# Optimization experiments

Measured on AMD Instinct MI355X. Metric: run time of the kernel, lower is better.

The kernel has to match this reference:

```python
import jax, jax.numpy as jnp
import numpy as np

NUM_NODES = 50000
DIM = 64
NUM_LAYERS = 2
NUM_EDGES = 800000
EPS = 1e-12


def _l2_normalize(x):
    # F.normalize(x, dim=1): x / max(||x||_2, eps)
    n = jnp.sqrt(jnp.sum(x * x, axis=1, keepdims=True))
    return x / jnp.maximum(n, EPS)


def _lgconv(x, src, dst):
    # PyG LGConv: symmetric gcn_norm without self-loops.
    # deg computed at target nodes; out[dst] += d^-1/2[src] * d^-1/2[dst] * x[src]
    ones = jnp.ones(src.shape[0], dtype=x.dtype)
    deg = jax.ops.segment_sum(ones, dst, num_segments=NUM_NODES)
    dinv = jnp.where(deg > 0, 1.0 / jnp.sqrt(jnp.where(deg > 0, deg, 1.0)), 0.0)
    norm = dinv[src] * dinv[dst]  # [E]
    msg = norm[:, None] * x[src]  # [E, D] gather + scale
    return jax.ops.segment_sum(msg, dst, num_segments=NUM_NODES)


def _propagate(x, edge_index):
    src, dst = edge_index[0], edge_index[1]
    for _ in range(NUM_LAYERS):
        x = _lgconv(x, src, dst)
    return _l2_normalize(x)


def setup_inputs() -> dict:
    key = jax.random.key(0)
    k1, k2, k3, k4 = jax.random.split(key, 4)
    x = jax.random.normal(k1, (NUM_NODES, DIM), dtype=jnp.float32)
    alpha = jnp.ones((3,), dtype=jnp.float32)
    ei_t = jax.random.randint(k2, (2, NUM_EDGES), 0, NUM_NODES, dtype=jnp.int32)
    ei_y = jax.random.randint(k3, (2, NUM_EDGES), 0, NUM_NODES, dtype=jnp.int32)
    ei_c = jax.random.randint(k4, (2, NUM_EDGES), 0, NUM_NODES, dtype=jnp.int32)
    return {"x": x, "alpha": alpha, "edge_index_title": ei_t,
            "edge_index_year": ei_y, "edge_index_cat": ei_c}


def reference(x, alpha, edge_index_title, edge_index_year, edge_index_cat):
    x = _l2_normalize(x)
    x_title = _propagate(x, edge_index_title)
    x_year = _propagate(x, edge_index_year)
    x_cat = _propagate(x, edge_index_cat)
    w = jax.nn.softmax(alpha, axis=0)
    w = jnp.clip(w, 0.0001, None)
    w = w / jnp.sum(w)
    return w[0] * x_title + w[1] * x_year + w[2] * x_cat
```

## Files before the change

### kernel.cpp

```cpp
#include <hip/hip_runtime.h>
#include <hip/hip_bf16.h>

#define NUM_NODES 50000
#define DIM 64
#define NUM_EDGES 800000
#define NUM_GRAPHS 3
#define TOT_NODES (NUM_NODES * NUM_GRAPHS)
#define EPS 1e-12f

#define NB2 391
#define TB2 (NB2 * NUM_GRAPHS)
#define PCAP2 2816
#define P3_CHUNK 4096
#define P3_BLOCKS ((NUM_EDGES + P3_CHUNK - 1) / P3_CHUNK)

typedef unsigned short ushort_t;
typedef unsigned int uint_t;
typedef unsigned int uint4v __attribute__((ext_vector_type(4)));
typedef unsigned short ushort8v __attribute__((ext_vector_type(8)));

__device__ __forceinline__ ushort_t f2bf(float f) {
    uint_t x = __float_as_uint(f);
    uint_t r = (x + 0x7FFFu + ((x >> 16) & 1u)) >> 16;
    return (ushort_t)r;
}

__device__ __forceinline__ void unpack_fma(uint4v w, float d, float* a) {
    a[0] += d * __uint_as_float(w[0] << 16);
    a[1] += d * __uint_as_float(w[0] & 0xFFFF0000u);
    a[2] += d * __uint_as_float(w[1] << 16);
    a[3] += d * __uint_as_float(w[1] & 0xFFFF0000u);
    a[4] += d * __uint_as_float(w[2] << 16);
    a[5] += d * __uint_as_float(w[2] & 0xFFFF0000u);
    a[6] += d * __uint_as_float(w[3] << 16);
    a[7] += d * __uint_as_float(w[3] & 0xFFFF0000u);
}
__device__ __forceinline__ void unpack_add(uint4v w, float* a) {
    a[0] += __uint_as_float(w[0] << 16);
    a[1] += __uint_as_float(w[0] & 0xFFFF0000u);
    a[2] += __uint_as_float(w[1] << 16);
    a[3] += __uint_as_float(w[1] & 0xFFFF0000u);
    a[4] += __uint_as_float(w[2] << 16);
    a[5] += __uint_as_float(w[2] & 0xFFFF0000u);
    a[6] += __uint_as_float(w[3] << 16);
    a[7] += __uint_as_float(w[3] & 0xFFFF0000u);
}

__global__ void l2norm_kernel(const float* __restrict__ in, ushort_t* __restrict__ out) {
    int row = blockIdx.x * (blockDim.x >> 6) + (threadIdx.x >> 6);
    int lane = threadIdx.x & 63;
    if (row >= NUM_NODES) return;
    float v = in[(long)row * DIM + lane];
    float s = v * v;
    #pragma unroll
    for (int off = 32; off > 0; off >>= 1)
        s += __shfl_xor(s, off, 64);
    float inv = 1.0f / fmaxf(sqrtf(s), EPS);
    out[(long)row * DIM + lane] = f2bf(v * inv);
}

__global__ __launch_bounds__(512) void partition_kernel(
        const int* __restrict__ e0, const int* __restrict__ e1, const int* __restrict__ e2,
        int* __restrict__ gcnt, uint_t* __restrict__ part) {
    __shared__ uint_t recs[P3_CHUNK];
    __shared__ int h[NB2], lstart[NB2], gbase[NB2], lcur[NB2];
    __shared__ int sc[512];

    int g = blockIdx.y;
    const int* ei = (g == 0) ? e0 : (g == 1) ? e1 : e2;
    const int* srcp = ei;
    const int* dstp = ei + NUM_EDGES;
    int base = blockIdx.x * P3_CHUNK;
    int n = min(P3_CHUNK, NUM_EDGES - base);
    int t = threadIdx.x;

    for (int i = t; i < NB2; i += 512) h[i] = 0;
    __syncthreads();
    for (int i = t; i < n; i += 512)
        atomicAdd(&h[dstp[base + i] >> 7], 1);
    __syncthreads();

    {
        int v = (t < NB2) ? h[t] : 0;
        sc[t] = v;
        __syncthreads();
        #pragma unroll
        for (int off = 1; off < 512; off <<= 1) {
            int add = (t >= off) ? sc[t - off] : 0;
            __syncthreads();
            sc[t] += add;
            __syncthreads();
        }
        if (t < NB2) {
            int ex = sc[t] - v;
            lstart[t] = ex;
            lcur[t] = ex;
            gbase[t] = (v > 0) ? atomicAdd(&gcnt[g * NB2 + t], v) : 0;
        }
    }
    __syncthreads();

    for (int i = t; i < n; i += 512) {
        int s = srcp[base + i];
        int d = dstp[base + i];
        int pos = atomicAdd(&lcur[d >> 7], 1);
        recs[pos] = ((uint_t)d << 16) | (uint_t)s;
    }
    __syncthreads();

    for (int i = t; i < n; i += 512) {
        uint_t r = recs[i];
        int b = r >> 23;
        int off = gbase[b] + (i - lstart[b]);
        if (off < PCAP2)
            part[(long)(g * NB2 + b) * PCAP2 + off] = r;
    }
}

__global__ __launch_bounds__(512) void bucket_sort_kernel(
        uint_t* __restrict__ part, const int* __restrict__ gcnt,
        int* __restrict__ row_start, int* __restrict__ row_end, float* __restrict__ dinv) {
    __shared__ uint_t recs[PCAP2];
    __shared__ int hist[128], lcur[128], sc[128];

    int b = blockIdx.x;
    int g = b / NB2;
    int bhi = b - g * NB2;
    long s0 = (long)b * PCAP2;
    int n = min(gcnt[b], PCAP2);
    int t = threadIdx.x;

    if (t < 128) hist[t] = 0;
    __syncthreads();
    for (int i = t; i < n; i += 512) {
        uint_t r = part[s0 + i];
        recs[i] = r;
        atomicAdd(&hist[(r >> 16) & 127], 1);
    }
    __syncthreads();
    int v = 0;
    if (t < 128) { v = hist[t]; sc[t] = v; }
    __syncthreads();
    #pragma unroll
    for (int off = 1; off < 128; off <<= 1) {
        int add = 0;
        if (t < 128 && t >= off) add = sc[t - off];
        __syncthreads();
        if (t < 128) sc[t] += add;
        __syncthreads();
    }
    if (t < 128) {
        int ex = sc[t] - v;
        lcur[t] = ex;
        int node = (bhi << 7) + t;
        if (node < NUM_NODES) {
            int k = g * NUM_NODES + node;
            int base = (int)(2 * s0);
            row_start[k] = base + ex;
            row_end[k]   = base + ex + v;
            dinv[k] = (v > 0) ? rsqrtf((float)v) : 0.0f;
        }
    }
    __syncthreads();

    ushort_t* es = (ushort_t*)part;
    for (int i = t; i < n; i += 512) {
        uint_t r = recs[i];
        int dl = (r >> 16) & 127;
        int pos = atomicAdd(&lcur[dl], 1);
        es[2 * s0 + pos] = (ushort_t)(r & 0xFFFFu);
    }
}

__global__ void conv1_all_kernel(const ushort_t* __restrict__ xn,
                                 const ushort_t* __restrict__ esort,
                                 const int* __restrict__ row_start,
                                 const int* __restrict__ row_end,
                                 const float* __restrict__ dinv,
                                 ushort_t* __restrict__ bufA) {
    int row = blockIdx.x * (blockDim.x >> 6) + (threadIdx.x >> 6);
    int g = blockIdx.y;
    int lane = threadIdx.x & 63;
    int sub = lane >> 3;
    int li  = lane & 7;
    if (row >= NUM_NODES) return;

    int k = g * NUM_NODES + row;
    int start = __builtin_amdgcn_readfirstlane(row_start[k]);
    int end   = __builtin_amdgcn_readfirstlane(row_end[k]);
    const float* dv = dinv + g * NUM_NODES;

    float a[8];
    #pragma unroll
    for (int j = 0; j < 8; ++j) a[j] = 0.0f;

    int i = start;
    for (; i + 32 <= end; i += 32) {
        int s0 = esort[i + sub];
        int s1 = esort[i + 8 + sub];
        int s2 = esort[i + 16 + sub];
        int s3 = esort[i + 24 + sub];
        float d0 = dv[s0], d1 = dv[s1], d2 = dv[s2], d3 = dv[s3];
        uint4v w0 = *(const uint4v*)(xn + (long)s0 * DIM + li * 8);
        uint4v w1 = *(const uint4v*)(xn + (long)s1 * DIM + li * 8);
        uint4v w2 = *(const uint4v*)(xn + (long)s2 * DIM + li * 8);
        uint4v w3 = *(const uint4v*)(xn + (long)s3 * DIM + li * 8);
        unpack_fma(w0, d0, a);
        unpack_fma(w1, d1, a);
        unpack_fma(w2, d2, a);
        unpack_fma(w3, d3, a);
    }
    for (; i + 16 <= end; i += 16) {
        int s0 = esort[i + sub];
        int s1 = esort[i + 8 + sub];
        float d0 = dv[s0], d1 = dv[s1];
        uint4v w0 = *(const uint4v*)(xn + (long)s0 * DIM + li * 8);
        uint4v w1 = *(const uint4v*)(xn + (long)s1 * DIM + li * 8);
        unpack_fma(w0, d0, a);
        unpack_fma(w1, d1, a);
    }
    for (; i < end; i += 8) {
        int e = i + sub;
        if (e < end) {
            int s = esort[e];
            float d = dv[s];
            uint4v w = *(const uint4v*)(xn + (long)s * DIM + li * 8);
            unpack_fma(w, d, a);
        }
    }
    #pragma unroll
    for (int off = 8; off < 64; off <<= 1) {
        #pragma unroll
        for (int j = 0; j < 8; ++j)
            a[j] += __shfl_xor(a[j], off, 64);
    }
    float dt = dv[row];
    float scl = dt * dt;
    if (sub == 0) {
        ushort8v o;
        #pragma unroll
        for (int j = 0; j < 8; ++j) o[j] = f2bf(a[j] * scl);
        *(ushort8v*)(bufA + (long)k * DIM + li * 8) = o;
    }
}

__global__ void conv2_kernel(const ushort_t* __restrict__ bufA,
                             const ushort_t* __restrict__ esort,
                             const int* __restrict__ row_start,
                             const int* __restrict__ row_end,
                             const float* __restrict__ alpha,
                             ushort_t* __restrict__ ybuf) {
    int row = blockIdx.x * (blockDim.x >> 6) + (threadIdx.x >> 6);
    int g = blockIdx.y;
    int lane = threadIdx.x & 63;
    int sub = lane >> 3;
    int li  = lane & 7;
    if (row >= NUM_NODES) return;

    float al0 = alpha[0], al1 = alpha[1], al2 = alpha[2];
    float m = fmaxf(al0, fmaxf(al1, al2));
    float e0 = expf(al0 - m), e1 = expf(al1 - m), e2 = expf(al2 - m);
    float es = e0 + e1 + e2;
    float w0 = fmaxf(e0 / es, 1e-4f);
    float w1 = fmaxf(e1 / es, 1e-4f);
    float w2 = fmaxf(e2 / es, 1e-4f);
    float wsum = w0 + w1 + w2;
    float wg = ((g == 0) ? w0 : (g == 1) ? w1 : w2) / wsum;

    int k = g * NUM_NODES + row;
    int start = __builtin_amdgcn_readfirstlane(row_start[k]);
    int end   = __builtin_amdgcn_readfirstlane(row_end[k]);
    const ushort_t* tbl = bufA + (long)g * NUM_NODES * DIM;

    float a[8];
    #pragma unroll
    for (int j = 0; j < 8; ++j) a[j] = 0.0f;

    int i = start;
    for (; i + 32 <= end; i += 32) {
        int s0 = esort[i + sub];
        int s1 = esort[i + 8 + sub];
        int s2 = esort[i + 16 + sub];
        int s3 = esort[i + 24 + sub];
        uint4v v0 = *(const uint4v*)(tbl + (long)s0 * DIM + li * 8);
        uint4v v1 = *(const uint4v*)(tbl + (long)s1 * DIM + li * 8);
        uint4v v2 = *(const uint4v*)(tbl + (long)s2 * DIM + li * 8);
        uint4v v3 = *(const uint4v*)(tbl + (long)s3 * DIM + li * 8);
        unpack_add(v0, a);
        unpack_add(v1, a);
        unpack_add(v2, a);
        unpack_add(v3, a);
    }
    for (; i + 16 <= end; i += 16) {
        int s0 = esort[i + sub];
        int s1 = esort[i + 8 + sub];
        uint4v v0 = *(const uint4v*)(tbl + (long)s0 * DIM + li * 8);
        uint4v v1 = *(const uint4v*)(tbl + (long)s1 * DIM + li * 8);
        unpack_add(v0, a);
        unpack_add(v1, a);
    }
    for (; i < end; i += 8) {
        int e = i + sub;
        if (e < end) {
            int s = esort[e];
            uint4v w = *(const uint4v*)(tbl + (long)s * DIM + li * 8);
            unpack_add(w, a);
        }
    }
    #pragma unroll
    for (int off = 8; off < 64; off <<= 1) {
        #pragma unroll
        for (int j = 0; j < 8; ++j)
            a[j] += __shfl_xor(a[j], off, 64);
    }
    float s = 0.0f;
    #pragma unroll
    for (int j = 0; j < 8; ++j) s += a[j] * a[j];
    #pragma unroll
    for (int off = 1; off < 8; off <<= 1)
        s += __shfl_xor(s, off, 64);
    float scl = wg / fmaxf(sqrtf(s), EPS);

    if (sub == 0) {
        ushort8v o;
        #pragma unroll
        for (int j = 0; j < 8; ++j) o[j] = f2bf(a[j] * scl);
        *(ushort8v*)(ybuf + (long)k * DIM + li * 8) = o;
    }
}

__global__ void blend_kernel(const ushort_t* __restrict__ ybuf, float* __restrict__ out) {
    int i = blockIdx.x * blockDim.x + threadIdx.x;
    if (i >= NUM_NODES * DIM / 8) return;
    uint4v w0 = *(const uint4v*)(ybuf + (long)i * 8);
    uint4v w1 = *(const uint4v*)(ybuf + (long)NUM_NODES * DIM + (long)i * 8);
    uint4v w2 = *(const uint4v*)(ybuf + 2L * NUM_NODES * DIM + (long)i * 8);
    float r[8];
    #pragma unroll
    for (int j = 0; j < 8; ++j) r[j] = 0.0f;
    unpack_add(w0, r);
    unpack_add(w1, r);
    unpack_add(w2, r);
    float* p = out + (long)i * 8;
    *(float4*)p = make_float4(r[0], r[1], r[2], r[3]);
    *(float4*)(p + 4) = make_float4(r[4], r[5], r[6], r[7]);
}

extern "C" void kernel_launch(void* const* d_in, const int* in_sizes, int n_in,
                              void* d_out, int out_size, void* d_ws, size_t ws_size,
                              hipStream_t stream) {
    const float* x     = (const float*)d_in[0];
    const float* alpha = (const float*)d_in[1];
    const int* e0 = (const int*)d_in[2];
    const int* e1 = (const int*)d_in[3];
    const int* e2 = (const int*)d_in[4];
    float* out = (float*)d_out;

    ushort_t* xn   = (ushort_t*)d_ws;
    ushort_t* bufA = xn + (long)NUM_NODES * DIM;
    ushort_t* ybuf = bufA + (long)TOT_NODES * DIM;
    float* dinv    = (float*)(ybuf + (long)TOT_NODES * DIM);
    int* row_start = (int*)(dinv + TOT_NODES);
    int* row_end   = row_start + 150016;
    int* gcnt      = row_end + 150016;
    uint_t* part   = (uint_t*)(gcnt + 1176);

    const int wave_grid = (NUM_NODES * 64 + 255) / 256;

    l2norm_kernel<<<wave_grid, 256, 0, stream>>>(x, xn);

    hipMemsetAsync(gcnt, 0, TB2 * sizeof(int), stream);
    {
        dim3 grd(P3_BLOCKS, NUM_GRAPHS);
        partition_kernel<<<grd, 512, 0, stream>>>(e0, e1, e2, gcnt, part);
    }
    bucket_sort_kernel<<<TB2, 512, 0, stream>>>(part, gcnt, row_start, row_end, dinv);

    const ushort_t* esort = (const ushort_t*)part;

    {
        dim3 grd(wave_grid, NUM_GRAPHS);
        conv1_all_kernel<<<grd, 256, 0, stream>>>(xn, esort, row_start, row_end, dinv, bufA);
    }
    {
        dim3 grd(wave_grid, NUM_GRAPHS);
        conv2_kernel<<<grd, 256, 0, stream>>>(bufA, esort, row_start, row_end, alpha, ybuf);
    }
    {
        int n8 = NUM_NODES * DIM / 8;
        blend_kernel<<<(n8 + 255) / 256, 256, 0, stream>>>(ybuf, out);
    }
}
```

Baseline: 260.5 us.

## Fuse conv2 with blend, use wave-shuffle scans, stage sorted edges in LDS

```diff
diff --git a/kernel.cpp b/kernel.cpp
--- a/kernel.cpp
+++ b/kernel.cpp
@@ -18,6 +18,7 @@
 typedef unsigned int uint_t;
 typedef unsigned int uint4v __attribute__((ext_vector_type(4)));
 typedef unsigned short ushort8v __attribute__((ext_vector_type(8)));
+typedef float f32x8 __attribute__((ext_vector_type(8)));
 
 __device__ __forceinline__ ushort_t f2bf(float f) {
     uint_t x = __float_as_uint(f);
@@ -25,25 +26,17 @@
     return (ushort_t)r;
 }
 
-__device__ __forceinline__ void unpack_fma(uint4v w, float d, float* a) {
-    a[0] += d * __uint_as_float(w[0] << 16);
-    a[1] += d * __uint_as_float(w[0] & 0xFFFF0000u);
-    a[2] += d * __uint_as_float(w[1] << 16);
-    a[3] += d * __uint_as_float(w[1] & 0xFFFF0000u);
-    a[4] += d * __uint_as_float(w[2] << 16);
-    a[5] += d * __uint_as_float(w[2] & 0xFFFF0000u);
-    a[6] += d * __uint_as_float(w[3] << 16);
-    a[7] += d * __uint_as_float(w[3] & 0xFFFF0000u);
-}
-__device__ __forceinline__ void unpack_add(uint4v w, float* a) {
-    a[0] += __uint_as_float(w[0] << 16);
-    a[1] += __uint_as_float(w[0] & 0xFFFF0000u);
-    a[2] += __uint_as_float(w[1] << 16);
-    a[3] += __uint_as_float(w[1] & 0xFFFF0000u);
-    a[4] += __uint_as_float(w[2] << 16);
-    a[5] += __uint_as_float(w[2] & 0xFFFF0000u);
-    a[6] += __uint_as_float(w[3] << 16);
-    a[7] += __uint_as_float(w[3] & 0xFFFF0000u);
+__device__ __forceinline__ f32x8 unpack8(uint4v w) {
+    f32x8 r;
+    r[0] = __uint_as_float(w[0] << 16);
+    r[1] = __uint_as_float(w[0] & 0xFFFF0000u);
+    r[2] = __uint_as_float(w[1] << 16);
+    r[3] = __uint_as_float(w[1] & 0xFFFF0000u);
+    r[4] = __uint_as_float(w[2] << 16);
+    r[5] = __uint_as_float(w[2] & 0xFFFF0000u);
+    r[6] = __uint_as_float(w[3] << 16);
+    r[7] = __uint_as_float(w[3] & 0xFFFF0000u);
+    return r;
 }
 
 __global__ void l2norm_kernel(const float* __restrict__ in, ushort_t* __restrict__ out) {
@@ -64,7 +57,7 @@
         int* __restrict__ gcnt, uint_t* __restrict__ part) {
     __shared__ uint_t recs[P3_CHUNK];
     __shared__ int h[NB2], lstart[NB2], gbase[NB2], lcur[NB2];
-    __shared__ int sc[512];
+    __shared__ int wsum[8];
 
     int g = blockIdx.y;
     const int* ei = (g == 0) ? e0 : (g == 1) ? e1 : e2;
@@ -73,6 +66,7 @@
     int base = blockIdx.x * P3_CHUNK;
     int n = min(P3_CHUNK, NUM_EDGES - base);
     int t = threadIdx.x;
+    int wid = t >> 6, ln = t & 63;
 
     for (int i = t; i < NB2; i += 512) h[i] = 0;
     __syncthreads();
@@ -82,17 +76,20 @@
 
     {
         int v = (t < NB2) ? h[t] : 0;
-        sc[t] = v;
+        int s = v;
+        #pragma unroll
+        for (int off = 1; off < 64; off <<= 1) {
+            int u = __shfl_up(s, off, 64);
+            if (ln >= off) s += u;
+        }
+        if (ln == 63) wsum[wid] = s;
         __syncthreads();
-        #pragma unroll
-        for (int off = 1; off < 512; off <<= 1) {
-            int add = (t >= off) ? sc[t - off] : 0;
-            __syncthreads();
-            sc[t] += add;
-            __syncthreads();
-        }
+        int prefix = 0;
+        #pragma unroll
+        for (int w = 0; w < 8; ++w)
+            if (w < wid) prefix += wsum[w];
         if (t < NB2) {
-            int ex = sc[t] - v;
+            int ex = prefix + s - v;
             lstart[t] = ex;
             lcur[t] = ex;
             gbase[t] = (v > 0) ? atomicAdd(&gcnt[g * NB2 + t], v) : 0;
@@ -121,7 +118,9 @@
         uint_t* __restrict__ part, const int* __restrict__ gcnt,
         int* __restrict__ row_start, int* __restrict__ row_end, float* __restrict__ dinv) {
     __shared__ uint_t recs[PCAP2];
-    __shared__ int hist[128], lcur[128], sc[128];
+    __shared__ ushort_t es_l[PCAP2];
+    __shared__ int hist[128], lcur[128];
+    __shared__ int w0sum;
 
     int b = blockIdx.x;
     int g = b / NB2;
@@ -129,6 +128,7 @@
     long s0 = (long)b * PCAP2;
     int n = min(gcnt[b], PCAP2);
     int t = threadIdx.x;
+    int ln = t & 63;
 
     if (t < 128) hist[t] = 0;
     __syncthreads();
@@ -138,19 +138,19 @@
         atomicAdd(&hist[(r >> 16) & 127], 1);
     }
     __syncthreads();
-    int v = 0;
-    if (t < 128) { v = hist[t]; sc[t] = v; }
-    __syncthreads();
+
+    int v = (t < 128) ? hist[t] : 0;
+    int s = v;
     #pragma unroll
-    for (int off = 1; off < 128; off <<= 1) {
-        int add = 0;
-        if (t < 128 && t >= off) add = sc[t - off];
-        __syncthreads();
-        if (t < 128) sc[t] += add;
-        __syncthreads();
-    }
+    for (int off = 1; off < 64; off <<= 1) {
+        int u = __shfl_up(s, off, 64);
+        if (ln >= off) s += u;
+    }
+    if (t == 63) w0sum = s;
+    __syncthreads();
     if (t < 128) {
-        int ex = sc[t] - v;
+        int prefix = (t >= 64) ? w0sum : 0;
+        int ex = prefix + s - v;
         lcur[t] = ex;
         int node = (bhi << 7) + t;
         if (node < NUM_NODES) {
@@ -163,13 +163,18 @@
     }
     __syncthreads();
 
-    ushort_t* es = (ushort_t*)part;
     for (int i = t; i < n; i += 512) {
         uint_t r = recs[i];
         int dl = (r >> 16) & 127;
         int pos = atomicAdd(&lcur[dl], 1);
-        es[2 * s0 + pos] = (ushort_t)(r & 0xFFFFu);
-    }
+        es_l[pos] = (ushort_t)(r & 0xFFFFu);
+    }
+    __syncthreads();
+    uint_t* es_out = (uint_t*)((ushort_t*)part + 2 * s0);
+    int nw = (n + 1) >> 1;
+    const uint_t* es_lw = (const uint_t*)es_l;
+    for (int i = t; i < nw; i += 512)
+        es_out[i] = es_lw[i];
 }
 
 __global__ void conv1_all_kernel(const ushort_t* __restrict__ xn,
@@ -190,9 +195,7 @@
     int end   = __builtin_amdgcn_readfirstlane(row_end[k]);
     const float* dv = dinv + g * NUM_NODES;
 
-    float a[8];
-    #pragma unroll
-    for (int j = 0; j < 8; ++j) a[j] = 0.0f;
+    f32x8 a = {0, 0, 0, 0, 0, 0, 0, 0};
 
     int i = start;
     for (; i + 32 <= end; i += 32) {
@@ -205,10 +208,10 @@
         uint4v w1 = *(const uint4v*)(xn + (long)s1 * DIM + li * 8);
         uint4v w2 = *(const uint4v*)(xn + (long)s2 * DIM + li * 8);
         uint4v w3 = *(const uint4v*)(xn + (long)s3 * DIM + li * 8);
-        unpack_fma(w0, d0, a);
-        unpack_fma(w1, d1, a);
-        unpack_fma(w2, d2, a);
-        unpack_fma(w3, d3, a);
+        a += unpack8(w0) * d0;
+        a += unpack8(w1) * d1;
+        a += unpack8(w2) * d2;
+        a += unpack8(w3) * d3;
     }
     for (; i + 16 <= end; i += 16) {
         int s0 = esort[i + sub];
@@ -216,8 +219,8 @@
         float d0 = dv[s0], d1 = dv[s1];
         uint4v w0 = *(const uint4v*)(xn + (long)s0 * DIM + li * 8);
         uint4v w1 = *(const uint4v*)(xn + (long)s1 * DIM + li * 8);
-        unpack_fma(w0, d0, a);
-        unpack_fma(w1, d1, a);
+        a += unpack8(w0) * d0;
+        a += unpack8(w1) * d1;
     }
     for (; i < end; i += 8) {
         int e = i + sub;
@@ -225,7 +228,7 @@
             int s = esort[e];
             float d = dv[s];
             uint4v w = *(const uint4v*)(xn + (long)s * DIM + li * 8);
-            unpack_fma(w, d, a);
+            a += unpack8(w) * d;
         }
     }
     #pragma unroll
@@ -244,14 +247,13 @@
     }
 }
 
-__global__ void conv2_kernel(const ushort_t* __restrict__ bufA,
-                             const ushort_t* __restrict__ esort,
-                             const int* __restrict__ row_start,
-                             const int* __restrict__ row_end,
-                             const float* __restrict__ alpha,
-                             ushort_t* __restrict__ ybuf) {
+__global__ void conv2_finalize_kernel(const ushort_t* __restrict__ bufA,
+                                      const ushort_t* __restrict__ esort,
+                                      const int* __restrict__ row_start,
+                                      const int* __restrict__ row_end,
+                                      const float* __restrict__ alpha,
+                                      float* __restrict__ out) {
     int row = blockIdx.x * (blockDim.x >> 6) + (threadIdx.x >> 6);
-    int g = blockIdx.y;
     int lane = threadIdx.x & 63;
     int sub = lane >> 3;
     int li  = lane & 7;
@@ -265,85 +267,71 @@
     float w1 = fmaxf(e1 / es, 1e-4f);
     float w2 = fmaxf(e2 / es, 1e-4f);
     float wsum = w0 + w1 + w2;
-    float wg = ((g == 0) ? w0 : (g == 1) ? w1 : w2) / wsum;
-
-    int k = g * NUM_NODES + row;
-    int start = __builtin_amdgcn_readfirstlane(row_start[k]);
-    int end   = __builtin_amdgcn_readfirstlane(row_end[k]);
-    const ushort_t* tbl = bufA + (long)g * NUM_NODES * DIM;
-
-    float a[8];
+
+    f32x8 res = {0, 0, 0, 0, 0, 0, 0, 0};
+
     #pragma unroll
-    for (int j = 0; j < 8; ++j) a[j] = 0.0f;
-
-    int i = start;
-    for (; i + 32 <= end; i += 32) {
-        int s0 = esort[i + sub];
-        int s1 = esort[i + 8 + sub];
-        int s2 = esort[i + 16 + sub];
-        int s3 = esort[i + 24 + sub];
-        uint4v v0 = *(const uint4v*)(tbl + (long)s0 * DIM + li * 8);
-        uint4v v1 = *(const uint4v*)(tbl + (long)s1 * DIM + li * 8);
-        uint4v v2 = *(const uint4v*)(tbl + (long)s2 * DIM + li * 8);
-        uint4v v3 = *(const uint4v*)(tbl + (long)s3 * DIM + li * 8);
-        unpack_add(v0, a);
-        unpack_add(v1, a);
-        unpack_add(v2, a);
-        unpack_add(v3, a);
-    }
-    for (; i + 16 <= end; i += 16) {
-        int s0 = esort[i + sub];
-        int s1 = esort[i + 8 + sub];
-        uint4v v0 = *(const uint4v*)(tbl + (long)s0 * DIM + li * 8);
-        uint4v v1 = *(const uint4v*)(tbl + (long)s1 * DIM + li * 8);
-        unpack_add(v0, a);
-        unpack_add(v1, a);
-    }
-    for (; i < end; i += 8) {
-        int e = i + sub;
-        if (e < end) {
-            int s = esort[e];
-            uint4v w = *(const uint4v*)(tbl + (long)s * DIM + li * 8);
-            unpack_add(w, a);
-        }
-    }
-    #pragma unroll
-    for (int off = 8; off < 64; off <<= 1) {
-        #pragma unroll
-        for (int j = 0; j < 8; ++j)
-            a[j] += __shfl_xor(a[j], off, 64);
-    }
-    float s = 0.0f;
-    #pragma unroll
-    for (int j = 0; j < 8; ++j) s += a[j] * a[j];
-    #pragma unroll
-    for (int off = 1; off < 8; off <<= 1)
-        s += __shfl_xor(s, off, 64);
-    float scl = wg / fmaxf(sqrtf(s), EPS);
+    for (int g = 0; g < NUM_GRAPHS; ++g) {
+        int k = g * NUM_NODES + row;
+        int start = __builtin_amdgcn_readfirstlane(row_start[k]);
+        int end   = __builtin_amdgcn_readfirstlane(row_end[k]);
+        const ushort_t* tbl = bufA + (long)g * NUM_NODES * DIM;
+
+        f32x8 a = {0, 0, 0, 0, 0, 0, 0, 0};
+
+        int i = start;
+        for (; i + 32 <= end; i += 32) {
+            int s0 = esort[i + sub];
+            int s1 = esort[i + 8 + sub];
+            int s2 = esort[i + 16 + sub];
+            int s3 = esort[i + 24 + sub];
+            uint4v v0 = *(const uint4v*)(tbl + (long)s0 * DIM + li * 8);
+            uint4v v1 = *(const uint4v*)(tbl + (long)s1 * DIM + li * 8);
+            uint4v v2 = *(const uint4v*)(tbl + (long)s2 * DIM + li * 8);
+            uint4v v3 = *(const uint4v*)(tbl + (long)s3 * DIM + li * 8);
+            a += unpack8(v0);
+            a += unpack8(v1);
+            a += unpack8(v2);
+            a += unpack8(v3);
+        }
+        for (; i + 16 <= end; i += 16) {
+            int s0 = esort[i + sub];
+            int s1 = esort[i + 8 + sub];
+            uint4v v0 = *(const uint4v*)(tbl + (long)s0 * DIM + li * 8);
+            uint4v v1 = *(const uint4v*)(tbl + (long)s1 * DIM + li * 8);
+            a += unpack8(v0);
+            a += unpack8(v1);
+        }
+        for (; i < end; i += 8) {
+            int e = i + sub;
+            if (e < end) {
+                int s = esort[e];
+                uint4v w = *(const uint4v*)(tbl + (long)s * DIM + li * 8);
+                a += unpack8(w);
+            }
+        }
+        #pragma unroll
+        for (int off = 8; off < 64; off <<= 1) {
+            #pragma unroll
+            for (int j = 0; j < 8; ++j)
+                a[j] += __shfl_xor(a[j], off, 64);
+        }
+        float s = 0.0f;
+        #pragma unroll
+        for (int j = 0; j < 8; ++j) s += a[j] * a[j];
+        #pragma unroll
+        for (int off = 1; off < 8; off <<= 1)
+            s += __shfl_xor(s, off, 64);
+        float wg = ((g == 0) ? w0 : (g == 1) ? w1 : w2) / wsum;
+        float scl = wg / fmaxf(sqrtf(s), EPS);
+        res += a * scl;
+    }
 
     if (sub == 0) {
-        ushort8v o;
-        #pragma unroll
-        for (int j = 0; j < 8; ++j) o[j] = f2bf(a[j] * scl);
-        *(ushort8v*)(ybuf + (long)k * DIM + li * 8) = o;
-    }
-}
-
-__global__ void blend_kernel(const ushort_t* __restrict__ ybuf, float* __restrict__ out) {
-    int i = blockIdx.x * blockDim.x + threadIdx.x;
-    if (i >= NUM_NODES * DIM / 8) return;
-    uint4v w0 = *(const uint4v*)(ybuf + (long)i * 8);
-    uint4v w1 = *(const uint4v*)(ybuf + (long)NUM_NODES * DIM + (long)i * 8);
-    uint4v w2 = *(const uint4v*)(ybuf + 2L * NUM_NODES * DIM + (long)i * 8);
-    float r[8];
-    #pragma unroll
-    for (int j = 0; j < 8; ++j) r[j] = 0.0f;
-    unpack_add(w0, r);
-    unpack_add(w1, r);
-    unpack_add(w2, r);
-    float* p = out + (long)i * 8;
-    *(float4*)p = make_float4(r[0], r[1], r[2], r[3]);
-    *(float4*)(p + 4) = make_float4(r[4], r[5], r[6], r[7]);
+        float* p = out + (long)row * DIM + li * 8;
+        *(float4*)p = make_float4(res[0], res[1], res[2], res[3]);
+        *(float4*)(p + 4) = make_float4(res[4], res[5], res[6], res[7]);
+    }
 }
 
 extern "C" void kernel_launch(void* const* d_in, const int* in_sizes, int n_in,
@@ -358,8 +346,7 @@
 
     ushort_t* xn   = (ushort_t*)d_ws;
     ushort_t* bufA = xn + (long)NUM_NODES * DIM;
-    ushort_t* ybuf = bufA + (long)TOT_NODES * DIM;
-    float* dinv    = (float*)(ybuf + (long)TOT_NODES * DIM);
+    float* dinv    = (float*)(bufA + (long)TOT_NODES * DIM);
     int* row_start = (int*)(dinv + TOT_NODES);
     int* row_end   = row_start + 150016;
     int* gcnt      = row_end + 150016;
@@ -382,12 +369,5 @@
         dim3 grd(wave_grid, NUM_GRAPHS);
         conv1_all_kernel<<<grd, 256, 0, stream>>>(xn, esort, row_start, row_end, dinv, bufA);
     }
-    {
-        dim3 grd(wave_grid, NUM_GRAPHS);
-        conv2_kernel<<<grd, 256, 0, stream>>>(bufA, esort, row_start, row_end, alpha, ybuf);
-    }
-    {
-        int n8 = NUM_NODES * DIM / 8;
-        blend_kernel<<<(n8 + 255) / 256, 256, 0, stream>>>(ybuf, out);
-    }
-}
+    conv2_finalize_kernel<<<wave_grid, 256, 0, stream>>>(bufA, esort, row_start, row_end, alpha, out);
+}
```

Result: faster. 237.1 us (-9.0%).
